# Kernel optimization log

Hardware: AMD Instinct MI355X
Metric: run time of the kernel (lower is better)

Reference implementation:

```python
import jax, jax.numpy as jnp
import numpy as np

C = 66  # channels (joints)
NB_CLASSES = 14
T = 96


def conv1d(x, w, b, pad, groups=1):
    # x: (N, Cin, L), w: (Cout, Cin//groups, K)
    y = jax.lax.conv_general_dilated(
        x, w, window_strides=(1,), padding=[(pad, pad)],
        feature_group_count=groups, dimension_numbers=('NCH', 'OIH', 'NCH'))
    return y + b[None, :, None]


def pool2(x):
    # AvgPool1d(kernel_size=2) along last axis
    return x.reshape(*x.shape[:-1], x.shape[-1] // 2, 2).mean(-1)


def setup_inputs() -> dict:
    key = jax.random.key(0)
    ks = jax.random.split(key, 16)

    def xavier(k, shape, fan_in, fan_out, gain=jnp.sqrt(2.0)):
        bound = gain * jnp.sqrt(6.0 / (fan_in + fan_out))
        return jax.random.uniform(k, shape, jnp.float32, -bound, bound)

    B = 2048
    x = jax.random.normal(ks[0], (B, T, C), jnp.float32)
    # shared convs (same weights for every channel)
    w_hs = xavier(ks[1], (8, 1, 7), 1 * 7, 8 * 7)
    b_hs = jnp.full((8,), 0.1, jnp.float32)
    w_ls = xavier(ks[2], (8, 1, 3), 1 * 3, 8 * 3)
    b_ls = jnp.full((8,), 0.1, jnp.float32)
    # per-channel individual convs, packed for grouped conv (groups=C)
    w_hi1 = xavier(ks[3], (C * 4, 8, 7), 8 * 7, 4 * 7)
    b_hi1 = jnp.full((C * 4,), 0.1, jnp.float32)
    w_hi2 = xavier(ks[4], (C * 4, 4, 7), 4 * 7, 4 * 7)
    b_hi2 = jnp.full((C * 4,), 0.1, jnp.float32)
    w_li1 = xavier(ks[5], (C * 4, 8, 3), 8 * 3, 4 * 3)
    b_li1 = jnp.full((C * 4,), 0.1, jnp.float32)
    w_li2 = xavier(ks[6], (C * 4, 4, 3), 4 * 3, 4 * 3)
    b_li2 = jnp.full((C * 4,), 0.1, jnp.float32)
    # MLP
    F_IN = 9 * C * 12
    w_fc1 = xavier(ks[7], (1936, F_IN), F_IN, 1936)
    b_fc1 = jnp.full((1936,), 0.1, jnp.float32)
    w_fc2 = xavier(ks[8], (NB_CLASSES, 1936), 1936, NB_CLASSES)
    b_fc2 = jnp.full((NB_CLASSES,), 0.1, jnp.float32)
    return dict(x=x, w_hs=w_hs, b_hs=b_hs, w_ls=w_ls, b_ls=b_ls,
                w_hi1=w_hi1, b_hi1=b_hi1, w_hi2=w_hi2, b_hi2=b_hi2,
                w_li1=w_li1, b_li1=b_li1, w_li2=w_li2, b_li2=b_li2,
                w_fc1=w_fc1, b_fc1=b_fc1, w_fc2=w_fc2, b_fc2=b_fc2)


def _branch(xc_flat, B, w_s, b_s, w_i1, b_i1, w_i2, b_i2, pad):
    # xc_flat: (B*C, 1, T). Shared conv applied per channel, then grouped
    # (per-channel) convs with groups=C.
    h = pool2(jax.nn.relu(conv1d(xc_flat, w_s, b_s, pad)))       # (B*C, 8, 48)
    h = h.reshape(B, C * 8, T // 2)
    h = pool2(jax.nn.relu(conv1d(h, w_i1, b_i1, pad, groups=C)))  # (B, C*4, 24)
    h = pool2(jax.nn.relu(conv1d(h, w_i2, b_i2, pad, groups=C)))  # (B, C*4, 12)
    return h.reshape(B, C, 4, T // 8)


def reference(x, w_hs, b_hs, w_ls, b_ls, w_hi1, b_hi1, w_hi2, b_hi2,
              w_li1, b_li1, w_li2, b_li2, w_fc1, b_fc1, w_fc2, b_fc2):
    B = x.shape[0]
    xc = jnp.transpose(x, (0, 2, 1))            # (B, C, T)
    xc_flat = xc.reshape(B * C, 1, T)
    high = _branch(xc_flat, B, w_hs, b_hs, w_hi1, b_hi1, w_hi2, b_hi2, pad=3)
    low = _branch(xc_flat, B, w_ls, b_ls, w_li1, b_li1, w_li2, b_li2, pad=1)
    orig = pool2(pool2(pool2(xc)))[:, :, None, :]  # (B, C, 1, 12)
    # per-channel concat order: [original, low, high] -> (B, C, 9, 12)
    feat = jnp.concatenate([orig, low, high], axis=2).reshape(B, 9 * C * 12)
    h = jax.nn.relu(feat @ w_fc1.T + b_fc1)
    return h @ w_fc2.T + b_fc2
```

## Files before the change

### kernel.cpp

```cpp
#include <hip/hip_runtime.h>
#include <hip/hip_bf16.h>

#define T_LEN 96
#define C_CH  66
#define FIN   7128
#define KPAD  7168
#define NFC1  1936
#define NPAD  2048
#define NCLS  14

typedef __bf16 bf16x8 __attribute__((ext_vector_type(8)));
typedef float  f32x4  __attribute__((ext_vector_type(4)));

#define GLD_LDS(gp, lp) __builtin_amdgcn_global_load_lds(                     \
    (__attribute__((address_space(1))) void*)(gp),                            \
    (__attribute__((address_space(3))) void*)(lp), 16, 0, 0)

__global__ __launch_bounds__(256) void transpose_kernel(
    const float* __restrict__ x, float* __restrict__ xT, int B)
{
    __shared__ float tile[64][65];
    const int t = threadIdx.x & 63;
    const int w = threadIdx.x >> 6;
    const int tc0 = blockIdx.x * 64;
    const int b0  = blockIdx.y * 64;
    #pragma unroll
    for (int j = 0; j < 16; j++) {
        const int r = w * 16 + j;
        tile[r][t] = x[(size_t)(b0 + r) * (T_LEN * C_CH) + tc0 + t];
    }
    __syncthreads();
    #pragma unroll
    for (int j = 0; j < 16; j++) {
        const int r = w * 16 + j;
        xT[(size_t)(tc0 + r) * B + b0 + t] = tile[t][r];
    }
}

__global__ __launch_bounds__(256) void pad_w_kernel(
    const float* __restrict__ w, __hip_bfloat16* __restrict__ wb)
{
    int idx = blockIdx.x * 256 + threadIdx.x;
    int row = idx / 896;
    int cc  = idx - row * 896;
    float4 a = {0.f, 0.f, 0.f, 0.f}, b = {0.f, 0.f, 0.f, 0.f};
    if (row < NFC1 && cc < 891) {
        const float4* src = (const float4*)(w + (size_t)row * FIN + cc * 8);
        a = src[0];
        b = src[1];
    }
    __align__(16) __hip_bfloat16 v[8];
    v[0] = __float2bfloat16(a.x); v[1] = __float2bfloat16(a.y);
    v[2] = __float2bfloat16(a.z); v[3] = __float2bfloat16(a.w);
    v[4] = __float2bfloat16(b.x); v[5] = __float2bfloat16(b.y);
    v[6] = __float2bfloat16(b.z); v[7] = __float2bfloat16(b.w);
    *(int4*)(wb + (size_t)row * KPAD + cc * 8) = *(const int4*)v;
}

template <int K, bool DO_EXTRA>
__global__ __launch_bounds__(64, 1) void conv_kernel(
    const float* __restrict__ x, int ts, int bs, int cs,
    const float* __restrict__ wS, const float* __restrict__ bS,
    const float* __restrict__ wI1, const float* __restrict__ bI1,
    const float* __restrict__ wI2, const float* __restrict__ bI2,
    __hip_bfloat16* __restrict__ feat, int out_off)
{
    constexpr int PAD = K / 2;
    const int lane = threadIdx.x;
    const int b = blockIdx.x * 64 + lane;
    const int c = blockIdx.y;

    const float* wi1 = wI1 + c * (4 * 8 * K);
    const float* bi1 = bI1 + c * 4;
    const float* wi2 = wI2 + c * (4 * 4 * K);
    const float* bi2 = bI2 + c * 4;

    float xh[T_LEN + 2 * PAD];
    #pragma unroll
    for (int i = 0; i < PAD; i++) { xh[i] = 0.f; xh[T_LEN + PAD + i] = 0.f; }
    const float* xb = x + (size_t)b * bs + (size_t)c * cs;
    #pragma unroll
    for (int t = 0; t < T_LEN; t++) xh[PAD + t] = xb[(size_t)t * ts];

    __hip_bfloat16* frow = feat + (size_t)b * KPAD + c * 108;

    if (DO_EXTRA) {
        #pragma unroll
        for (int q = 0; q < 12; q++) {
            float s = 0.f;
            #pragma unroll
            for (int k = 0; k < 8; k++) s += xh[PAD + q * 8 + k];
            frow[q] = __float2bfloat16(s * 0.125f);
        }
        if (c == 0) {
            int4* tail = (int4*)(feat + (size_t)b * KPAD + FIN);
            const int4 z = {0, 0, 0, 0};
            #pragma unroll
            for (int i = 0; i < 5; i++) tail[i] = z;
        }
    }

    float s2a[4 * 48];
    #pragma unroll
    for (int oc = 0; oc < 4; oc++) {
        const float bv = bi1[oc];
        #pragma unroll
        for (int p = 0; p < 48; p++) s2a[oc * 48 + p] = bv;
    }

    #pragma unroll 1
    for (int ic = 0; ic < 8; ic++) {
        float ws[K];
        #pragma unroll
        for (int k = 0; k < K; k++) ws[k] = wS[ic * K + k];
        const float bs1 = bS[ic];

        float th[48 + 2 * PAD];
        #pragma unroll
        for (int i = 0; i < PAD; i++) { th[i] = 0.f; th[48 + PAD + i] = 0.f; }
        #pragma unroll
        for (int p = 0; p < 48; p++) {
            float y0 = bs1, y1 = bs1;
            #pragma unroll
            for (int k = 0; k < K; k++) {
                y0 = fmaf(ws[k], xh[2 * p + k], y0);
                y1 = fmaf(ws[k], xh[2 * p + 1 + k], y1);
            }
            th[PAD + p] = 0.5f * (fmaxf(y0, 0.f) + fmaxf(y1, 0.f));
        }

        float wv0[K], wv1[K], wv2[K], wv3[K];
        #pragma unroll
        for (int k = 0; k < K; k++) {
            wv0[k] = wi1[(0 * 8 + ic) * K + k];
            wv1[k] = wi1[(1 * 8 + ic) * K + k];
            wv2[k] = wi1[(2 * 8 + ic) * K + k];
            wv3[k] = wi1[(3 * 8 + ic) * K + k];
        }
        #pragma unroll
        for (int p = 0; p < 48; p++) {
            float a0 = s2a[0 * 48 + p], a1 = s2a[1 * 48 + p];
            float a2 = s2a[2 * 48 + p], a3 = s2a[3 * 48 + p];
            #pragma unroll
            for (int k = 0; k < K; k++) {
                const float t = th[p + k];
                a0 = fmaf(wv0[k], t, a0);
                a1 = fmaf(wv1[k], t, a1);
                a2 = fmaf(wv2[k], t, a2);
                a3 = fmaf(wv3[k], t, a3);
            }
            s2a[0 * 48 + p] = a0; s2a[1 * 48 + p] = a1;
            s2a[2 * 48 + p] = a2; s2a[3 * 48 + p] = a3;
        }
    }

    float s2ph[4][24 + 2 * PAD];
    #pragma unroll
    for (int ic = 0; ic < 4; ic++) {
        #pragma unroll
        for (int i = 0; i < PAD; i++) {
            s2ph[ic][i] = 0.f; s2ph[ic][24 + PAD + i] = 0.f;
        }
        #pragma unroll
        for (int q = 0; q < 24; q++)
            s2ph[ic][PAD + q] = 0.5f * (fmaxf(s2a[ic * 48 + 2 * q], 0.f) +
                                        fmaxf(s2a[ic * 48 + 2 * q + 1], 0.f));
    }

    #pragma unroll 1
    for (int oc = 0; oc < 4; oc++) {
        const float bv = bi2[oc];
        #pragma unroll
        for (int q = 0; q < 12; q++) {
            float y0 = bv, y1 = bv;
            #pragma unroll
            for (int ic = 0; ic < 4; ic++) {
                #pragma unroll
                for (int k = 0; k < K; k++) {
                    const float w = wi2[(oc * 4 + ic) * K + k];
                    y0 = fmaf(w, s2ph[ic][2 * q + k], y0);
                    y1 = fmaf(w, s2ph[ic][2 * q + 1 + k], y1);
                }
            }
            frow[out_off + oc * 12 + q] =
                __float2bfloat16(0.5f * (fmaxf(y0, 0.f) + fmaxf(y1, 0.f)));
        }
    }
}

__global__ __launch_bounds__(256) void gemm_kernel(
    const __hip_bfloat16* __restrict__ A,
    const __hip_bfloat16* __restrict__ Bw,
    float* __restrict__ Cm, int kchunk)
{
    __shared__ __align__(16) __hip_bfloat16 As[4096];
    __shared__ __align__(16) __hip_bfloat16 Bs[4096];

    const int tid  = threadIdx.x;
    const int lane = tid & 63;
    const int wid  = tid >> 6;
    const int m0 = blockIdx.y * 128;
    const int n0 = blockIdx.x * 128;
    const int wm = (wid >> 1) * 64;
    const int wn = (wid & 1) * 64;
    const int lr = lane & 15;
    const int quad = lane >> 4;

    const int r0 = tid >> 2, c0 = (tid & 3) * 8;
    const __hip_bfloat16* gA0 = A  + (size_t)(m0 + r0) * KPAD + c0;
    const __hip_bfloat16* gA1 = gA0 + (size_t)64 * KPAD;
    const __hip_bfloat16* gB0 = Bw + (size_t)(n0 + r0) * KPAD + c0;
    const __hip_bfloat16* gB1 = gB0 + (size_t)64 * KPAD;
    __hip_bfloat16* lA0 = As + wid * 512;
    __hip_bfloat16* lA1 = As + 2048 + wid * 512;
    __hip_bfloat16* lB0 = Bs + wid * 512;
    __hip_bfloat16* lB1 = Bs + 2048 + wid * 512;

    f32x4 acc[4][4] = {};

    const int kBeg = blockIdx.z * kchunk;
    const int kEnd = kBeg + kchunk;
    for (int k0 = kBeg; k0 < kEnd; k0 += 32) {
        __syncthreads();
        GLD_LDS(gA0 + k0, lA0);
        GLD_LDS(gA1 + k0, lA1);
        GLD_LDS(gB0 + k0, lB0);
        GLD_LDS(gB1 + k0, lB1);
        __syncthreads();
        bf16x8 af[4], bfr[4];
        #pragma unroll
        for (int mt = 0; mt < 4; mt++)
            af[mt] = *(const bf16x8*)(As + (wm + mt * 16 + lr) * 32 + quad * 8);
        #pragma unroll
        for (int nt = 0; nt < 4; nt++)
            bfr[nt] = *(const bf16x8*)(Bs + (wn + nt * 16 + lr) * 32 + quad * 8);
        #pragma unroll
        for (int mt = 0; mt < 4; mt++)
            #pragma unroll
            for (int nt = 0; nt < 4; nt++)
                acc[mt][nt] = __builtin_amdgcn_mfma_f32_16x16x32_bf16(
                    af[mt], bfr[nt], acc[mt][nt], 0, 0, 0);
    }

    float* Cs = Cm + (size_t)blockIdx.z * NPAD * NPAD;
    #pragma unroll
    for (int mt = 0; mt < 4; mt++) {
        #pragma unroll
        for (int nt = 0; nt < 4; nt++) {
            const int col = n0 + wn + nt * 16 + lr;
            const int rb  = m0 + wm + mt * 16 + quad * 4;
            #pragma unroll
            for (int r = 0; r < 4; r++)
                Cs[(size_t)(rb + r) * NPAD + col] = acc[mt][nt][r];
        }
    }
}

__global__ __launch_bounds__(256) void fc2_kernel(
    const float* __restrict__ h1, const float* __restrict__ b1,
    const float* __restrict__ w2, const float* __restrict__ b2,
    float* __restrict__ out, int nslab)
{
    const int b = blockIdx.x;
    const int tid = threadIdx.x;
    float acc[NCLS];
    #pragma unroll
    for (int o = 0; o < NCLS; o++) acc[o] = 0.f;
    for (int n = tid; n < NFC1; n += 256) {
        float hv = b1[n];
        for (int s = 0; s < nslab; s++)
            hv += h1[(size_t)s * NPAD * NPAD + (size_t)b * NPAD + n];
        float h = fmaxf(hv, 0.f);
        #pragma unroll
        for (int o = 0; o < NCLS; o++)
            acc[o] = fmaf(h, w2[o * NFC1 + n], acc[o]);
    }
    __shared__ float red[4][NCLS];
    #pragma unroll
    for (int o = 0; o < NCLS; o++) {
        float v = acc[o];
        #pragma unroll
        for (int s = 32; s > 0; s >>= 1) v += __shfl_down(v, s);
        if ((tid & 63) == 0) red[tid >> 6][o] = v;
    }
    __syncthreads();
    if (tid < NCLS)
        out[b * NCLS + tid] = red[0][tid] + red[1][tid] + red[2][tid] +
                              red[3][tid] + b2[tid];
}

extern "C" void kernel_launch(void* const* d_in, const int* in_sizes, int n_in,
                              void* d_out, int out_size, void* d_ws, size_t ws_size,
                              hipStream_t stream)
{
    (void)n_in; (void)out_size;
    const float* x     = (const float*)d_in[0];
    const float* w_hs  = (const float*)d_in[1];
    const float* b_hs  = (const float*)d_in[2];
    const float* w_ls  = (const float*)d_in[3];
    const float* b_ls  = (const float*)d_in[4];
    const float* w_hi1 = (const float*)d_in[5];
    const float* b_hi1 = (const float*)d_in[6];
    const float* w_hi2 = (const float*)d_in[7];
    const float* b_hi2 = (const float*)d_in[8];
    const float* w_li1 = (const float*)d_in[9];
    const float* b_li1 = (const float*)d_in[10];
    const float* w_li2 = (const float*)d_in[11];
    const float* b_li2 = (const float*)d_in[12];
    const float* w_fc1 = (const float*)d_in[13];
    const float* b_fc1 = (const float*)d_in[14];
    const float* w_fc2 = (const float*)d_in[15];
    const float* b_fc2 = (const float*)d_in[16];
    float* out = (float*)d_out;

    const int B = in_sizes[0] / (T_LEN * C_CH);

    char* ws = (char*)d_ws;
    const size_t featB = (size_t)B * KPAD * 2;
    const size_t wbB   = (size_t)NPAD * KPAD * 2;
    const size_t slabB = (size_t)NPAD * NPAD * 4;
    const size_t xtB   = (size_t)T_LEN * C_CH * B * 4;
    const size_t base2 = featB + wbB;

    __hip_bfloat16* feat = (__hip_bfloat16*)ws;
    __hip_bfloat16* wb   = (__hip_bfloat16*)(ws + featB);
    float* h1            = (float*)(ws + base2);

    const int sk = (ws_size >= base2 + 4 * slabB) ? 4 : 2;
    const bool use_xt = (ws_size >= base2 + sk * slabB + xtB);
    float* xT = (float*)(ws + base2 + sk * slabB);

    pad_w_kernel<<<dim3((NPAD * 896) / 256), 256, 0, stream>>>(w_fc1, wb);

    const float* cx = x;
    int ts = C_CH, bsi = T_LEN * C_CH, cs = 1;
    if (use_xt) {
        transpose_kernel<<<dim3(99, B / 64), 256, 0, stream>>>(x, xT, B);
        cx = xT; ts = C_CH * B; bsi = 1; cs = B;
    }
    conv_kernel<7, false><<<dim3(B / 64, C_CH), 64, 0, stream>>>(
        cx, ts, bsi, cs, w_hs, b_hs, w_hi1, b_hi1, w_hi2, b_hi2, feat, 60);
    conv_kernel<3, true><<<dim3(B / 64, C_CH), 64, 0, stream>>>(
        cx, ts, bsi, cs, w_ls, b_ls, w_li1, b_li1, w_li2, b_li2, feat, 12);
    gemm_kernel<<<dim3(NPAD / 128, B / 128, sk), 256, 0, stream>>>(
        feat, wb, h1, KPAD / sk);
    fc2_kernel<<<dim3(B), 256, 0, stream>>>(h1, b_fc1, w_fc2, b_fc2, out, sk);
}
```

Before: 472.1 us.

## Tile conv branches over time windows and fuse both branches into one launch

Each conv branch now runs over four 24-sample time windows with halos instead of holding the full 96-sample input and 4x48 stage-2 accumulators in registers. Recomputing the halo lets each thread hold far fewer registers, so launch bounds rise to two waves per SIMD for more occupancy. The high and low branches now run in a single launch that uses grid z to pick the branch, which removes one kernel launch. In exchange, the halo input loads and shared-conv outputs are recomputed at window edges, and the second conv stage adds boundary checks.

Result: faster. 431.2 us (-8.7%).

```diff
diff --git a/kernel.cpp b/kernel.cpp
--- a/kernel.cpp
+++ b/kernel.cpp
@@ -58,113 +58,83 @@
 }
 
 template <int K, bool DO_EXTRA>
-__global__ __launch_bounds__(64, 1) void conv_kernel(
-    const float* __restrict__ x, int ts, int bs, int cs,
+__device__ __forceinline__ void conv_branch(
+    const float* __restrict__ xb, int ts,
     const float* __restrict__ wS, const float* __restrict__ bS,
-    const float* __restrict__ wI1, const float* __restrict__ bI1,
-    const float* __restrict__ wI2, const float* __restrict__ bI2,
-    __hip_bfloat16* __restrict__ feat, int out_off)
+    const float* __restrict__ wi1, const float* __restrict__ bi1,
+    const float* __restrict__ wi2, const float* __restrict__ bi2,
+    __hip_bfloat16* __restrict__ frow, int out_off)
 {
     constexpr int PAD = K / 2;
-    const int lane = threadIdx.x;
-    const int b = blockIdx.x * 64 + lane;
-    const int c = blockIdx.y;
-
-    const float* wi1 = wI1 + c * (4 * 8 * K);
-    const float* bi1 = bI1 + c * 4;
-    const float* wi2 = wI2 + c * (4 * 4 * K);
-    const float* bi2 = bI2 + c * 4;
-
-    float xh[T_LEN + 2 * PAD];
-    #pragma unroll
-    for (int i = 0; i < PAD; i++) { xh[i] = 0.f; xh[T_LEN + PAD + i] = 0.f; }
-    const float* xb = x + (size_t)b * bs + (size_t)c * cs;
-    #pragma unroll
-    for (int t = 0; t < T_LEN; t++) xh[PAD + t] = xb[(size_t)t * ts];
-
-    __hip_bfloat16* frow = feat + (size_t)b * KPAD + c * 108;
-
-    if (DO_EXTRA) {
-        #pragma unroll
-        for (int q = 0; q < 12; q++) {
-            float s = 0.f;
-            #pragma unroll
-            for (int k = 0; k < 8; k++) s += xh[PAD + q * 8 + k];
-            frow[q] = __float2bfloat16(s * 0.125f);
-        }
-        if (c == 0) {
-            int4* tail = (int4*)(feat + (size_t)b * KPAD + FIN);
-            const int4 z = {0, 0, 0, 0};
-            #pragma unroll
-            for (int i = 0; i < 5; i++) tail[i] = z;
-        }
-    }
-
-    float s2a[4 * 48];
-    #pragma unroll
-    for (int oc = 0; oc < 4; oc++) {
-        const float bv = bi1[oc];
-        #pragma unroll
-        for (int p = 0; p < 48; p++) s2a[oc * 48 + p] = bv;
-    }
-
-    #pragma unroll 1
-    for (int ic = 0; ic < 8; ic++) {
-        float ws[K];
-        #pragma unroll
-        for (int k = 0; k < K; k++) ws[k] = wS[ic * K + k];
-        const float bs1 = bS[ic];
-
-        float th[48 + 2 * PAD];
-        #pragma unroll
-        for (int i = 0; i < PAD; i++) { th[i] = 0.f; th[48 + PAD + i] = 0.f; }
-        #pragma unroll
-        for (int p = 0; p < 48; p++) {
-            float y0 = bs1, y1 = bs1;
-            #pragma unroll
-            for (int k = 0; k < K; k++) {
-                y0 = fmaf(ws[k], xh[2 * p + k], y0);
-                y1 = fmaf(ws[k], xh[2 * p + 1 + k], y1);
+    constexpr int XW  = 24 + 6 * PAD;
+    constexpr int THW = 12 + 2 * PAD;
+
+    float s2phR[4][24];
+
+    #pragma unroll
+    for (int tt = 0; tt < 4; tt++) {
+        float xw[XW];
+        #pragma unroll
+        for (int i = 0; i < XW; i++) {
+            const int t = 24 * tt - 3 * PAD + i;
+            xw[i] = (t >= 0 && t < T_LEN) ? xb[(size_t)t * ts] : 0.f;
+        }
+
+        if (DO_EXTRA) {
+            #pragma unroll
+            for (int r = 0; r < 3; r++) {
+                float s = 0.f;
+                #pragma unroll
+                for (int k = 0; k < 8; k++) s += xw[3 * PAD + 8 * r + k];
+                frow[3 * tt + r] = __float2bfloat16(s * 0.125f);
             }
-            th[PAD + p] = 0.5f * (fmaxf(y0, 0.f) + fmaxf(y1, 0.f));
-        }
-
-        float wv0[K], wv1[K], wv2[K], wv3[K];
-        #pragma unroll
-        for (int k = 0; k < K; k++) {
-            wv0[k] = wi1[(0 * 8 + ic) * K + k];
-            wv1[k] = wi1[(1 * 8 + ic) * K + k];
-            wv2[k] = wi1[(2 * 8 + ic) * K + k];
-            wv3[k] = wi1[(3 * 8 + ic) * K + k];
-        }
-        #pragma unroll
-        for (int p = 0; p < 48; p++) {
-            float a0 = s2a[0 * 48 + p], a1 = s2a[1 * 48 + p];
-            float a2 = s2a[2 * 48 + p], a3 = s2a[3 * 48 + p];
-            #pragma unroll
-            for (int k = 0; k < K; k++) {
-                const float t = th[p + k];
-                a0 = fmaf(wv0[k], t, a0);
-                a1 = fmaf(wv1[k], t, a1);
-                a2 = fmaf(wv2[k], t, a2);
-                a3 = fmaf(wv3[k], t, a3);
+        }
+
+        float s2a[4][12];
+        #pragma unroll
+        for (int oc = 0; oc < 4; oc++) {
+            const float bv = bi1[oc];
+            #pragma unroll
+            for (int q = 0; q < 12; q++) s2a[oc][q] = bv;
+        }
+
+        #pragma unroll 1
+        for (int ic = 0; ic < 8; ic++) {
+            const float bs1 = bS[ic];
+            float thw[THW];
+            #pragma unroll
+            for (int j = 0; j < THW; j++) {
+                const int jg = 12 * tt - PAD + j;
+                if (jg < 0 || jg >= 48) { thw[j] = 0.f; continue; }
+                float y0 = bs1, y1 = bs1;
+                #pragma unroll
+                for (int k = 0; k < K; k++) {
+                    const float w = wS[ic * K + k];
+                    y0 = fmaf(w, xw[2 * j + k], y0);
+                    y1 = fmaf(w, xw[2 * j + 1 + k], y1);
+                }
+                thw[j] = 0.5f * (fmaxf(y0, 0.f) + fmaxf(y1, 0.f));
             }
-            s2a[0 * 48 + p] = a0; s2a[1 * 48 + p] = a1;
-            s2a[2 * 48 + p] = a2; s2a[3 * 48 + p] = a3;
-        }
-    }
-
-    float s2ph[4][24 + 2 * PAD];
-    #pragma unroll
-    for (int ic = 0; ic < 4; ic++) {
-        #pragma unroll
-        for (int i = 0; i < PAD; i++) {
-            s2ph[ic][i] = 0.f; s2ph[ic][24 + PAD + i] = 0.f;
-        }
-        #pragma unroll
-        for (int q = 0; q < 24; q++)
-            s2ph[ic][PAD + q] = 0.5f * (fmaxf(s2a[ic * 48 + 2 * q], 0.f) +
-                                        fmaxf(s2a[ic * 48 + 2 * q + 1], 0.f));
+            #pragma unroll
+            for (int q = 0; q < 12; q++) {
+                #pragma unroll
+                for (int oc = 0; oc < 4; oc++) {
+                    float a = s2a[oc][q];
+                    #pragma unroll
+                    for (int k = 0; k < K; k++)
+                        a = fmaf(wi1[(oc * 8 + ic) * K + k], thw[q + k], a);
+                    s2a[oc][q] = a;
+                }
+            }
+        }
+
+        #pragma unroll
+        for (int oc = 0; oc < 4; oc++)
+            #pragma unroll
+            for (int r = 0; r < 6; r++)
+                s2phR[oc][6 * tt + r] =
+                    0.5f * (fmaxf(s2a[oc][2 * r], 0.f) +
+                            fmaxf(s2a[oc][2 * r + 1], 0.f));
     }
 
     #pragma unroll 1
@@ -178,13 +148,48 @@
                 #pragma unroll
                 for (int k = 0; k < K; k++) {
                     const float w = wi2[(oc * 4 + ic) * K + k];
-                    y0 = fmaf(w, s2ph[ic][2 * q + k], y0);
-                    y1 = fmaf(w, s2ph[ic][2 * q + 1 + k], y1);
+                    const int i0 = 2 * q + k - PAD;
+                    const int i1 = 2 * q + 1 + k - PAD;
+                    if (i0 >= 0 && i0 < 24) y0 = fmaf(w, s2phR[ic][i0], y0);
+                    if (i1 >= 0 && i1 < 24) y1 = fmaf(w, s2phR[ic][i1], y1);
                 }
             }
             frow[out_off + oc * 12 + q] =
                 __float2bfloat16(0.5f * (fmaxf(y0, 0.f) + fmaxf(y1, 0.f)));
         }
+    }
+}
+
+__global__ __launch_bounds__(64, 2) void conv_fused_kernel(
+    const float* __restrict__ x, int ts, int bs, int cs,
+    const float* __restrict__ w_hs, const float* __restrict__ b_hs,
+    const float* __restrict__ w_ls, const float* __restrict__ b_ls,
+    const float* __restrict__ w_hi1, const float* __restrict__ b_hi1,
+    const float* __restrict__ w_hi2, const float* __restrict__ b_hi2,
+    const float* __restrict__ w_li1, const float* __restrict__ b_li1,
+    const float* __restrict__ w_li2, const float* __restrict__ b_li2,
+    __hip_bfloat16* __restrict__ feat)
+{
+    const int lane = threadIdx.x;
+    const int b = blockIdx.x * 64 + lane;
+    const int c = blockIdx.y;
+    const float* xb = x + (size_t)b * bs + (size_t)c * cs;
+    __hip_bfloat16* frow = feat + (size_t)b * KPAD + c * 108;
+
+    if (blockIdx.z == 0) {
+        conv_branch<7, false>(xb, ts, w_hs, b_hs,
+                              w_hi1 + c * 224, b_hi1 + c * 4,
+                              w_hi2 + c * 112, b_hi2 + c * 4, frow, 60);
+    } else {
+        if (c == 0) {
+            int4* tail = (int4*)(feat + (size_t)b * KPAD + FIN);
+            const int4 z = {0, 0, 0, 0};
+            #pragma unroll
+            for (int i = 0; i < 5; i++) tail[i] = z;
+        }
+        conv_branch<3, true>(xb, ts, w_ls, b_ls,
+                             w_li1 + c * 96, b_li1 + c * 4,
+                             w_li2 + c * 48, b_li2 + c * 4, frow, 12);
     }
 }
 
@@ -338,10 +343,9 @@
         transpose_kernel<<<dim3(99, B / 64), 256, 0, stream>>>(x, xT, B);
         cx = xT; ts = C_CH * B; bsi = 1; cs = B;
     }
-    conv_kernel<7, false><<<dim3(B / 64, C_CH), 64, 0, stream>>>(
-        cx, ts, bsi, cs, w_hs, b_hs, w_hi1, b_hi1, w_hi2, b_hi2, feat, 60);
-    conv_kernel<3, true><<<dim3(B / 64, C_CH), 64, 0, stream>>>(
-        cx, ts, bsi, cs, w_ls, b_ls, w_li1, b_li1, w_li2, b_li2, feat, 12);
+    conv_fused_kernel<<<dim3(B / 64, C_CH, 2), 64, 0, stream>>>(
+        cx, ts, bsi, cs, w_hs, b_hs, w_ls, b_ls,
+        w_hi1, b_hi1, w_hi2, b_hi2, w_li1, b_li1, w_li2, b_li2, feat);
     gemm_kernel<<<dim3(NPAD / 128, B / 128, sk), 256, 0, stream>>>(
         feat, wb, h1, KPAD / sk);
     fc2_kernel<<<dim3(B), 256, 0, stream>>>(h1, b_fc1, w_fc2, b_fc2, out, sk);
```
